# Kernel tuning notes

Hardware: AMD Instinct MI355X
Metric: run time of the kernel (lower is better)

The kernel has to match this reference:

```python
import jax, jax.numpy as jnp
import numpy as np

N_JOINTS = 24

def _rodrigues(r):
    # r: [B, J, 3] axis-angle -> [B, J, 3, 3] rotation matrices
    theta = jnp.clip(jnp.linalg.norm(r, axis=-1, keepdims=True), 1e-6)  # [B,J,1]
    rh = r / theta
    z = jnp.zeros_like(rh[..., :1])
    # skew-symmetric matrix m
    m = jnp.stack([
        jnp.concatenate([z, -rh[..., 2:3], rh[..., 1:2]], -1),
        jnp.concatenate([rh[..., 2:3], z, -rh[..., 0:1]], -1),
        jnp.concatenate([-rh[..., 1:2], rh[..., 0:1], z], -1),
    ], axis=-2)  # [B,J,3,3]
    rrT = rh[..., :, None] * rh[..., None, :]  # outer product [B,J,3,3]
    cos = jnp.cos(theta)[..., None]
    sin = jnp.sin(theta)[..., None]
    eye = jnp.eye(3, dtype=r.dtype)
    return cos * eye + (1.0 - cos) * rrT + sin * m

def _with_zeros(Rm, t):
    # Rm: [B,3,3], t: [B,3] -> [B,4,4] homogeneous transform
    B = Rm.shape[0]
    top = jnp.concatenate([Rm, t[:, :, None]], axis=-1)  # [B,3,4]
    bot = jnp.broadcast_to(jnp.array([0.0, 0.0, 0.0, 1.0], Rm.dtype), (B, 1, 4))
    return jnp.concatenate([top, bot], axis=1)

def _keypoints(v, idx):
    # v: [B,N,3], idx: [G,K] vertex-index groups -> [B,G,3] via (max+min)/2
    g = v[:, idx]  # [B,G,K,3] irregular gather
    return (g.max(axis=2) + g.min(axis=2)) * 0.5

def setup_inputs() -> dict:
    key = jax.random.key(0)
    ks = jax.random.split(key, 8)
    B, N, P, K = 64, 40000, 100, 128
    beta = jax.random.normal(ks[0], (B, P), jnp.float32)
    pose = jax.random.normal(ks[1], (B, N_JOINTS * 3), jnp.float32) * 0.3
    trans = jax.random.normal(ks[2], (B, 3), jnp.float32)
    shapedirs = jax.random.normal(ks[3], (P, 3 * N), jnp.float32) * 0.01
    v_template = jax.random.normal(ks[4], (N, 3), jnp.float32)
    w = jax.random.uniform(ks[5], (N, N_JOINTS), jnp.float32)
    weights = w / w.sum(axis=1, keepdims=True)  # LBS weights sum to 1
    reorder_index = jnp.arange(N_JOINTS, dtype=jnp.int64 if jax.config.jax_enable_x64 else jnp.int32)
    # kinematic tree: parent[i] < i (binary-tree shape stands in for the rabbit skeleton)
    parent = jnp.concatenate([jnp.zeros(1, jnp.int32), (jnp.arange(1, N_JOINTS, dtype=jnp.int32) - 1) // 2])
    joint_idx = jax.random.randint(ks[6], (N_JOINTS - 1, K), 0, N)
    add_idx = jax.random.randint(ks[7], (7, K), 0, N)
    return {"beta": beta, "pose": pose, "trans": trans, "shapedirs": shapedirs,
            "v_template": v_template, "weights": weights, "reorder_index": reorder_index,
            "parent": parent, "joint_idx": joint_idx, "add_idx": add_idx}

def reference(beta, pose, trans, shapedirs, v_template, weights,
              reorder_index, parent, joint_idx, add_idx):
    B = beta.shape[0]
    pose = pose.reshape(B, N_JOINTS, 3)[:, reorder_index]
    # blend shapes: v_shaped = beta @ shapedirs + template
    v_posed = (beta @ shapedirs + v_template.reshape(-1)).reshape(B, -1, 3)  # [B,N,3]
    # joints from vertex-group (max+min)/2, root is zero
    J = jnp.concatenate([jnp.zeros((B, 1, 3), beta.dtype), _keypoints(v_posed, joint_idx)], axis=1)  # [B,24,3]
    R = _rodrigues(pose)  # [B,24,3,3]
    # forward kinematics along the tree (fixed 24-joint loop)
    par = np.asarray(jax.device_get(parent))
    G = [_with_zeros(R[:, 0], J[:, 0])]
    for i in range(1, N_JOINTS):
        p = int(par[i])
        G_loc = _with_zeros(R[:, i], J[:, i] - J[:, p])
        G.append(jnp.matmul(G[p], G_loc))
    G = jnp.stack(G, axis=1)  # [B,24,4,4]
    # remove rest-pose joint locations (pack subtraction only touches last column)
    Jh = jnp.concatenate([J, jnp.zeros((B, N_JOINTS, 1), beta.dtype)], axis=-1)[..., None]  # [B,24,4,1]
    t_corr = jnp.matmul(G, Jh)  # [B,24,4,1]
    G1 = jnp.concatenate([G[..., :3], G[..., 3:4] - t_corr], axis=-1)
    # LBS skinning: per-vertex blended transform
    T = jnp.einsum('nk,bkij->bnij', weights, G1)  # [B,N,4,4]
    vh = jnp.concatenate([v_posed, jnp.ones((B, v_posed.shape[1], 1), beta.dtype)], axis=-1)  # [B,N,4]
    posed = jnp.einsum('bnij,bnj->bni', T, vh)[..., :3] + trans[:, None, :]  # [B,N,3]
    skeleton = jnp.concatenate([
        jnp.zeros((B, 1, 3), beta.dtype),
        _keypoints(posed, joint_idx),
        _keypoints(posed, add_idx),
    ], axis=1)  # [B,31,3]
    return posed, skeleton
```

## Files before the change

### kernel.cpp

```cpp
#include <hip/hip_runtime.h>
#include <math.h>

#define B   64
#define NV  40000
#define P   100
#define KG  128
#define NJ  24
#define TV  16
#define NSK 31
#define NSUB (KG / TV)

typedef __attribute__((ext_vector_type(8))) short bf16x8;
typedef __attribute__((ext_vector_type(4))) float f32x4;

__device__ __forceinline__ unsigned short rne_bf16(float f) {
  unsigned u = __float_as_uint(f);
  u = (u + 0x7FFFu + ((u >> 16) & 1u)) >> 16;
  return (unsigned short)u;
}

__global__ void k_prep(const float* __restrict__ beta,
                       unsigned short* __restrict__ beta_bf) {
  const int t = blockIdx.x * 256 + threadIdx.x;
  if (t < B * 136) {
    const int m = t / 136, k = t % 136;
    beta_bf[t] = (k < P) ? rne_bf16(beta[m * P + k]) : (unsigned short)0;
  }
}

__global__ __launch_bounds__(256)
void k_jpart(const unsigned short* __restrict__ beta_bf,
             const float* __restrict__ sd,
             const float* __restrict__ vt,
             const int*   __restrict__ joint_idx,
             float*       __restrict__ pmn,
             float*       __restrict__ pmx) {
  const int j = blockIdx.x;
  const int s = blockIdx.y;
  const int t = threadIdx.x;
  const int lane = t & 63, wv = t >> 6;
  const int l15 = lane & 15, qd = lane >> 4;

  __shared__ __align__(16) unsigned short sdT_s[48 * 136];
  __shared__ __align__(16) float pos_s[64 * 68];
  __shared__ float vt_s[48];
  __shared__ int   idx_s[TV];

  if (t < TV) idx_s[t] = joint_idx[j * KG + s * TV + t];
  __syncthreads();

  for (int task = t; task < 768; task += 256) {
    const int n = task % 48, kg = task / 48;
    const size_t colbase = (size_t)idx_s[n / 3] * 3 + (n % 3);
    unsigned pk[4];
#pragma unroll
    for (int h = 0; h < 4; ++h) {
      const int k0 = kg * 8 + 2 * h;
      float f0 = 0.0f, f1 = 0.0f;
      if (k0 < P)     f0 = sd[(size_t)k0 * (3 * NV) + colbase];
      if (k0 + 1 < P) f1 = sd[(size_t)(k0 + 1) * (3 * NV) + colbase];
      pk[h] = (unsigned)rne_bf16(f0) | ((unsigned)rne_bf16(f1) << 16);
    }
    *(uint4*)&sdT_s[n * 136 + kg * 8] = make_uint4(pk[0], pk[1], pk[2], pk[3]);
  }
  if (t < 48) vt_s[t] = vt[(size_t)idx_s[t / 3] * 3 + (t % 3)];
  __syncthreads();

  f32x4 acc[3];
#pragma unroll
  for (int nt = 0; nt < 3; ++nt) acc[nt] = (f32x4){0.f, 0.f, 0.f, 0.f};
#pragma unroll
  for (int ks = 0; ks < 4; ++ks) {
    const bf16x8 af = *(const bf16x8*)&beta_bf[(wv * 16 + l15) * 136 + ks * 32 + qd * 8];
#pragma unroll
    for (int nt = 0; nt < 3; ++nt) {
      const bf16x8 bf = *(const bf16x8*)&sdT_s[(nt * 16 + l15) * 136 + ks * 32 + qd * 8];
      acc[nt] = __builtin_amdgcn_mfma_f32_16x16x32_bf16(af, bf, acc[nt], 0, 0, 0);
    }
  }
  float vtv[3];
#pragma unroll
  for (int nt = 0; nt < 3; ++nt) vtv[nt] = vt_s[nt * 16 + l15];

#pragma unroll
  for (int nt = 0; nt < 3; ++nt) {
    const int n = nt * 16 + l15;
    const int v = n / 3, c = n - 3 * v;
#pragma unroll
    for (int r = 0; r < 4; ++r) {
      const int m = wv * 16 + qd * 4 + r;
      pos_s[m * 68 + v * 4 + c] = acc[nt][r] + vtv[nt];
    }
  }
  __syncthreads();

  if (t < 192) {
    const int b = t / 3, c = t % 3;
    float lo = 1e30f, hi = -1e30f;
#pragma unroll
    for (int v = 0; v < TV; ++v) {
      const float val = pos_s[b * 68 + v * 4 + c];
      lo = fminf(lo, val); hi = fmaxf(hi, val);
    }
    pmn[((j * NSUB + s) * B + b) * 3 + c] = lo;
    pmx[((j * NSUB + s) * B + b) * 3 + c] = hi;
  }
}

__global__ void k_chain(const float* __restrict__ pose,
                        const int*   __restrict__ parent,
                        const float* __restrict__ pmn,
                        const float* __restrict__ pmx,
                        const float* __restrict__ trans,
                        unsigned short* __restrict__ G1A) {
  const int b = blockIdx.x;
  const int t = threadIdx.x;

  __shared__ float R[NJ][9];
  __shared__ float Jl[NJ][3];
  __shared__ float G[NJ][12];
  __shared__ float G1c[NJ][12];

  if (t < NJ) {
    const float x = pose[b * NJ * 3 + t * 3 + 0];
    const float y = pose[b * NJ * 3 + t * 3 + 1];
    const float z = pose[b * NJ * 3 + t * 3 + 2];
    const float th = fmaxf(sqrtf(x * x + y * y + z * z), 1e-6f);
    const float xh = x / th, yh = y / th, zh = z / th;
    const float c = cosf(th), s = sinf(th), o = 1.0f - c;
    R[t][0] = c + o * xh * xh;      R[t][1] = o * xh * yh - s * zh; R[t][2] = o * xh * zh + s * yh;
    R[t][3] = o * xh * yh + s * zh; R[t][4] = c + o * yh * yh;      R[t][5] = o * yh * zh - s * xh;
    R[t][6] = o * xh * zh - s * yh; R[t][7] = o * yh * zh + s * xh; R[t][8] = c + o * zh * zh;
    if (t == 0) {
      Jl[0][0] = 0.0f; Jl[0][1] = 0.0f; Jl[0][2] = 0.0f;
    } else {
      const int jj = t - 1;
#pragma unroll
      for (int c2 = 0; c2 < 3; ++c2) {
        float lo = 1e30f, hi = -1e30f;
#pragma unroll
        for (int s2 = 0; s2 < NSUB; ++s2) {
          lo = fminf(lo, pmn[((jj * NSUB + s2) * B + b) * 3 + c2]);
          hi = fmaxf(hi, pmx[((jj * NSUB + s2) * B + b) * 3 + c2]);
        }
        Jl[t][c2] = 0.5f * (lo + hi);
      }
    }
  }
  __syncthreads();

  if (t < 12) {
    const int r = t >> 2, c = t & 3;
    G[0][t] = (c < 3) ? R[0][r * 3 + c] : Jl[0][r];
  }
  __syncthreads();

  for (int i = 1; i < NJ; ++i) {
    const int p = parent[i];
    if (t < 12) {
      const int r = t >> 2, c = t & 3;
      const float g0 = G[p][r * 4 + 0];
      const float g1 = G[p][r * 4 + 1];
      const float g2 = G[p][r * 4 + 2];
      float l0, l1, l2, add;
      if (c < 3) {
        l0 = R[i][0 * 3 + c]; l1 = R[i][1 * 3 + c]; l2 = R[i][2 * 3 + c];
        add = 0.0f;
      } else {
        l0 = Jl[i][0] - Jl[p][0]; l1 = Jl[i][1] - Jl[p][1]; l2 = Jl[i][2] - Jl[p][2];
        add = G[p][r * 4 + 3];
      }
      G[i][t] = g0 * l0 + g1 * l1 + g2 * l2 + add;
    }
    __syncthreads();
  }

  for (int e = t; e < NJ * 12; e += 64) {
    const int i = e / 12, rc = e % 12, r = rc >> 2, c = rc & 3;
    float val;
    if (c < 3) {
      val = G[i][rc];
    } else {
      val = G[i][r * 4 + 3] - (G[i][r * 4 + 0] * Jl[i][0] +
                               G[i][r * 4 + 1] * Jl[i][1] +
                               G[i][r * 4 + 2] * Jl[i][2]);
    }
    G1c[i][rc] = val;
  }
  __syncthreads();

  for (int e = t; e < 512; e += 64) {
    const int m = e >> 5, k = e & 31;
    float val = 0.0f;
    if (m < 12) {
      if (k < NJ) val = G1c[k][m];
      else if (k == NJ && (m & 3) == 3) val = trans[b * 3 + (m >> 2)];
    }
    G1A[(size_t)b * 512 + e] = rne_bf16(val);
  }
}

__global__ __launch_bounds__(256)
void k_skin(const float* __restrict__ sd,
            const float* __restrict__ vt,
            const float* __restrict__ w,
            const unsigned short* __restrict__ beta_bf,
            const unsigned short* __restrict__ G1A,
            float*       __restrict__ out) {
  const int n0v = blockIdx.x * TV;
  const int col0 = n0v * 3;
  const int t  = threadIdx.x;
  const int lane = t & 63, wv = t >> 6;
  const int l15 = lane & 15, q = lane >> 4;

  __shared__ __align__(16) float vhf[64 * 68];

  f32x4 acc[3];
#pragma unroll
  for (int nt = 0; nt < 3; ++nt) acc[nt] = (f32x4){0.f, 0.f, 0.f, 0.f};
#pragma unroll
  for (int ks = 0; ks < 4; ++ks) {
    const bf16x8 af = *(const bf16x8*)&beta_bf[(wv * 16 + l15) * 136 + ks * 32 + q * 8];
#pragma unroll
    for (int nt = 0; nt < 3; ++nt) {
      float bv[8];
#pragma unroll
      for (int jj = 0; jj < 8; ++jj) {
        const int k = ks * 32 + q * 8 + jj;
        if (ks < 3) {
          bv[jj] = sd[(size_t)k * (3 * NV) + col0 + nt * 16 + l15];
        } else {
          bv[jj] = (k < P) ? sd[(size_t)k * (3 * NV) + col0 + nt * 16 + l15] : 0.0f;
        }
      }
      bf16x8 bfr;
#pragma unroll
      for (int jj = 0; jj < 8; ++jj) bfr[jj] = (short)rne_bf16(bv[jj]);
      acc[nt] = __builtin_amdgcn_mfma_f32_16x16x32_bf16(af, bfr, acc[nt], 0, 0, 0);
    }
  }
  float vtv[3];
#pragma unroll
  for (int nt = 0; nt < 3; ++nt) vtv[nt] = vt[col0 + nt * 16 + l15];

#pragma unroll
  for (int nt = 0; nt < 3; ++nt) {
    const int n = nt * 16 + l15;
    const int v = n / 3, c = n - 3 * v;
#pragma unroll
    for (int r = 0; r < 4; ++r) {
      const int m = wv * 16 + q * 4 + r;
      vhf[m * 68 + v * 4 + c] = acc[nt][r] + vtv[nt];
    }
  }
  __syncthreads();

  bf16x8 wf;
  if (q < 3) {
    const float* wrow = &w[(size_t)(n0v + l15) * NJ + q * 8];
    const float4 w0 = *(const float4*)wrow;
    const float4 w1 = *(const float4*)(wrow + 4);
    wf[0] = (short)rne_bf16(w0.x); wf[1] = (short)rne_bf16(w0.y);
    wf[2] = (short)rne_bf16(w0.z); wf[3] = (short)rne_bf16(w0.w);
    wf[4] = (short)rne_bf16(w1.x); wf[5] = (short)rne_bf16(w1.y);
    wf[6] = (short)rne_bf16(w1.z); wf[7] = (short)rne_bf16(w1.w);
  } else {
    wf = (bf16x8){0, 0, 0, 0, 0, 0, 0, 0};
    wf[0] = (short)0x3F80;
  }
  const f32x4 zero = (f32x4){0.f, 0.f, 0.f, 0.f};
#pragma unroll 4
  for (int bi = 0; bi < 16; ++bi) {
    const int b = wv * 16 + bi;
    const bf16x8 gf = *(const bf16x8*)&G1A[(size_t)b * 512 + l15 * 32 + q * 8];
    const f32x4 d = __builtin_amdgcn_mfma_f32_16x16x32_bf16(gf, wf, zero, 0, 0, 0);
    const float4 vh = *(const float4*)&vhf[b * 68 + l15 * 4];
    if (q < 3) {
      out[(size_t)b * (NV * 3) + col0 + l15 * 3 + q] =
          d[0] * vh.x + d[1] * vh.y + d[2] * vh.z + d[3];
    }
  }
}

__global__ void k_skel(const float* __restrict__ posed,
                       const int*   __restrict__ joint_idx,
                       const int*   __restrict__ add_idx,
                       float*       __restrict__ skel) {
  const int j = blockIdx.x;
  const int b = blockIdx.y;
  const int t = threadIdx.x;
  const int idx = (j < 23) ? joint_idx[j * KG + t] : add_idx[(j - 23) * KG + t];

  const float* p = posed + (size_t)b * NV * 3 + (size_t)idx * 3;
  float mn[3], mx[3];
#pragma unroll
  for (int c = 0; c < 3; ++c) { mn[c] = p[c]; mx[c] = p[c]; }
#pragma unroll
  for (int off = 32; off > 0; off >>= 1) {
#pragma unroll
    for (int c = 0; c < 3; ++c) {
      mn[c] = fminf(mn[c], __shfl_down(mn[c], off));
      mx[c] = fmaxf(mx[c], __shfl_down(mx[c], off));
    }
  }
  __shared__ float s_mn[2][3], s_mx[2][3];
  const int wave = t >> 6, lane = t & 63;
  if (lane == 0) {
#pragma unroll
    for (int c = 0; c < 3; ++c) { s_mn[wave][c] = mn[c]; s_mx[wave][c] = mx[c]; }
  }
  __syncthreads();
  if (t == 0) {
#pragma unroll
    for (int c = 0; c < 3; ++c) {
      float lo = fminf(s_mn[0][c], s_mn[1][c]);
      float hi = fmaxf(s_mx[0][c], s_mx[1][c]);
      skel[(b * NSK + 1 + j) * 3 + c] = 0.5f * (lo + hi);
      if (j == 0) skel[(b * NSK + 0) * 3 + c] = 0.0f;
    }
  }
}

extern "C" void kernel_launch(void* const* d_in, const int* in_sizes, int n_in,
                              void* d_out, int out_size, void* d_ws, size_t ws_size,
                              hipStream_t stream) {
  const float* beta     = (const float*)d_in[0];
  const float* pose     = (const float*)d_in[1];
  const float* trans    = (const float*)d_in[2];
  const float* sd       = (const float*)d_in[3];
  const float* vt       = (const float*)d_in[4];
  const float* w        = (const float*)d_in[5];
  const int* parent     = (const int*)d_in[7];
  const int* joint_idx  = (const int*)d_in[8];
  const int* add_idx    = (const int*)d_in[9];

  float* out = (float*)d_out;
  unsigned short* G1A     = (unsigned short*)d_ws;
  unsigned short* beta_bf = G1A + B * 512;
  float* pmn = (float*)(beta_bf + B * 136);
  float* pmx = pmn + 23 * NSUB * B * 3;

  k_prep <<<(B * 136 + 255) / 256, 256, 0, stream>>>(beta, beta_bf);
  k_jpart<<<dim3(23, NSUB), 256, 0, stream>>>(beta_bf, sd, vt, joint_idx, pmn, pmx);
  k_chain<<<B, 64, 0, stream>>>(pose, parent, pmn, pmx, trans, G1A);
  k_skin <<<NV / TV, 256, 0, stream>>>(sd, vt, w, beta_bf, G1A, out);
  k_skel <<<dim3(30, B), 128, 0, stream>>>(out, joint_idx, add_idx,
                                           out + (size_t)B * NV * 3);
}
```

Before: 158.4 us.

## Fold beta bf16 prep into k_jpart and stage shapedirs tiles in LDS for skinning

New measurement: 160.7 us. No clear change (+1.5%).

```diff
diff --git a/kernel.cpp b/kernel.cpp
--- a/kernel.cpp
+++ b/kernel.cpp
@@ -19,22 +19,14 @@
   return (unsigned short)u;
 }
 
-__global__ void k_prep(const float* __restrict__ beta,
-                       unsigned short* __restrict__ beta_bf) {
-  const int t = blockIdx.x * 256 + threadIdx.x;
-  if (t < B * 136) {
-    const int m = t / 136, k = t % 136;
-    beta_bf[t] = (k < P) ? rne_bf16(beta[m * P + k]) : (unsigned short)0;
-  }
-}
-
 __global__ __launch_bounds__(256)
-void k_jpart(const unsigned short* __restrict__ beta_bf,
+void k_jpart(const float* __restrict__ beta,
              const float* __restrict__ sd,
              const float* __restrict__ vt,
              const int*   __restrict__ joint_idx,
              float*       __restrict__ pmn,
-             float*       __restrict__ pmx) {
+             float*       __restrict__ pmx,
+             unsigned short* __restrict__ beta_bf) {
   const int j = blockIdx.x;
   const int s = blockIdx.y;
   const int t = threadIdx.x;
@@ -47,35 +39,50 @@
   __shared__ int   idx_s[TV];
 
   if (t < TV) idx_s[t] = joint_idx[j * KG + s * TV + t];
-  __syncthreads();
-
-  for (int task = t; task < 768; task += 256) {
-    const int n = task % 48, kg = task / 48;
-    const size_t colbase = (size_t)idx_s[n / 3] * 3 + (n % 3);
-    unsigned pk[4];
-#pragma unroll
-    for (int h = 0; h < 4; ++h) {
-      const int k0 = kg * 8 + 2 * h;
-      float f0 = 0.0f, f1 = 0.0f;
-      if (k0 < P)     f0 = sd[(size_t)k0 * (3 * NV) + colbase];
-      if (k0 + 1 < P) f1 = sd[(size_t)(k0 + 1) * (3 * NV) + colbase];
-      pk[h] = (unsigned)rne_bf16(f0) | ((unsigned)rne_bf16(f1) << 16);
-    }
-    *(uint4*)&sdT_s[n * 136 + kg * 8] = make_uint4(pk[0], pk[1], pk[2], pk[3]);
+
+  if (j == 0 && s == 0) {
+    for (int e = t; e < B * 136; e += 256) {
+      const int m = e / 136, k = e % 136;
+      beta_bf[e] = (k < P) ? rne_bf16(beta[m * P + k]) : (unsigned short)0;
+    }
+  }
+  __syncthreads();
+
+  for (int e = t; e < 48 * 28; e += 256) {
+    const int n = e / 28, k = P + e % 28;
+    sdT_s[n * 136 + k] = 0;
+  }
+  for (int task = t; task < TV * P; task += 256) {
+    const int v = task / P, k = task % P;
+    const float* src = sd + (size_t)k * (3 * NV) + (size_t)idx_s[v] * 3;
+    const float f0 = src[0], f1 = src[1], f2 = src[2];
+    sdT_s[(v * 3 + 0) * 136 + k] = rne_bf16(f0);
+    sdT_s[(v * 3 + 1) * 136 + k] = rne_bf16(f1);
+    sdT_s[(v * 3 + 2) * 136 + k] = rne_bf16(f2);
   }
   if (t < 48) vt_s[t] = vt[(size_t)idx_s[t / 3] * 3 + (t % 3)];
   __syncthreads();
 
+  const int m0 = wv * 16 + l15;
+  bf16x8 af[4];
+#pragma unroll
+  for (int ks = 0; ks < 4; ++ks) {
+#pragma unroll
+    for (int jj = 0; jj < 8; ++jj) {
+      const int k = ks * 32 + qd * 8 + jj;
+      af[ks][jj] = (short)((k < P) ? rne_bf16(beta[m0 * P + k]) : (unsigned short)0);
+    }
+  }
+
   f32x4 acc[3];
 #pragma unroll
   for (int nt = 0; nt < 3; ++nt) acc[nt] = (f32x4){0.f, 0.f, 0.f, 0.f};
 #pragma unroll
   for (int ks = 0; ks < 4; ++ks) {
-    const bf16x8 af = *(const bf16x8*)&beta_bf[(wv * 16 + l15) * 136 + ks * 32 + qd * 8];
 #pragma unroll
     for (int nt = 0; nt < 3; ++nt) {
       const bf16x8 bf = *(const bf16x8*)&sdT_s[(nt * 16 + l15) * 136 + ks * 32 + qd * 8];
-      acc[nt] = __builtin_amdgcn_mfma_f32_16x16x32_bf16(af, bf, acc[nt], 0, 0, 0);
+      acc[nt] = __builtin_amdgcn_mfma_f32_16x16x32_bf16(af[ks], bf, acc[nt], 0, 0, 0);
     }
   }
   float vtv[3];
@@ -213,7 +220,23 @@
   const int lane = t & 63, wv = t >> 6;
   const int l15 = lane & 15, q = lane >> 4;
 
+  __shared__ __align__(16) unsigned short sdT_s[48 * 136];
   __shared__ __align__(16) float vhf[64 * 68];
+
+  for (int task = t; task < 768; task += 256) {
+    const int n = task % 48, kg = task / 48;
+    unsigned pk[4];
+#pragma unroll
+    for (int h = 0; h < 4; ++h) {
+      const int k0 = kg * 8 + 2 * h;
+      float f0 = 0.0f, f1 = 0.0f;
+      if (k0 < P)     f0 = sd[(size_t)k0 * (3 * NV) + col0 + n];
+      if (k0 + 1 < P) f1 = sd[(size_t)(k0 + 1) * (3 * NV) + col0 + n];
+      pk[h] = (unsigned)rne_bf16(f0) | ((unsigned)rne_bf16(f1) << 16);
+    }
+    *(uint4*)&sdT_s[n * 136 + kg * 8] = make_uint4(pk[0], pk[1], pk[2], pk[3]);
+  }
+  __syncthreads();
 
   f32x4 acc[3];
 #pragma unroll
@@ -223,20 +246,8 @@
     const bf16x8 af = *(const bf16x8*)&beta_bf[(wv * 16 + l15) * 136 + ks * 32 + q * 8];
 #pragma unroll
     for (int nt = 0; nt < 3; ++nt) {
-      float bv[8];
-#pragma unroll
-      for (int jj = 0; jj < 8; ++jj) {
-        const int k = ks * 32 + q * 8 + jj;
-        if (ks < 3) {
-          bv[jj] = sd[(size_t)k * (3 * NV) + col0 + nt * 16 + l15];
-        } else {
-          bv[jj] = (k < P) ? sd[(size_t)k * (3 * NV) + col0 + nt * 16 + l15] : 0.0f;
-        }
-      }
-      bf16x8 bfr;
-#pragma unroll
-      for (int jj = 0; jj < 8; ++jj) bfr[jj] = (short)rne_bf16(bv[jj]);
-      acc[nt] = __builtin_amdgcn_mfma_f32_16x16x32_bf16(af, bfr, acc[nt], 0, 0, 0);
+      const bf16x8 bf = *(const bf16x8*)&sdT_s[(nt * 16 + l15) * 136 + ks * 32 + q * 8];
+      acc[nt] = __builtin_amdgcn_mfma_f32_16x16x32_bf16(af, bf, acc[nt], 0, 0, 0);
     }
   }
   float vtv[3];
@@ -340,8 +351,8 @@
   float* pmn = (float*)(beta_bf + B * 136);
   float* pmx = pmn + 23 * NSUB * B * 3;
 
-  k_prep <<<(B * 136 + 255) / 256, 256, 0, stream>>>(beta, beta_bf);
-  k_jpart<<<dim3(23, NSUB), 256, 0, stream>>>(beta_bf, sd, vt, joint_idx, pmn, pmx);
+  k_jpart<<<dim3(23, NSUB), 256, 0, stream>>>(beta, sd, vt, joint_idx,
+                                              pmn, pmx, beta_bf);
   k_chain<<<B, 64, 0, stream>>>(pose, parent, pmn, pmx, trans, G1A);
   k_skin <<<NV / TV, 256, 0, stream>>>(sd, vt, w, beta_bf, G1A, out);
   k_skel <<<dim3(30, B), 128, 0, stream>>>(out, joint_idx, add_idx,
```
